# Kernel tuning notes

Hardware: AMD Instinct MI355X
Metric: run time of the kernel (lower is better)

The kernel has to match this reference:

```python
import jax, jax.numpy as jnp
import numpy as np

B, C_IN, C_OUT, H, W, OH, OW, K = 2, 8, 16, 512, 1024, 512, 1024, 9


def setup_inputs() -> dict:
    key = jax.random.key(0)
    k1, k2, k3, k4 = jax.random.split(key, 4)
    x = jax.random.normal(k1, (B, C_IN, H, W), dtype=jnp.float32)
    # sample_map holds (x, y) float pixel coords; scale rand [0,1) into bounds
    sm = jax.random.uniform(k2, (OH, OW, K, 2), dtype=jnp.float32)
    sample_map = sm * jnp.array([W - 1.0, H - 1.0], dtype=jnp.float32)
    n = C_IN * K
    stdv = 1.0 / np.sqrt(n)
    weight = jax.random.uniform(k3, (C_OUT, C_IN, K), dtype=jnp.float32,
                                minval=-stdv, maxval=stdv)
    bias = jax.random.uniform(k4, (C_OUT,), dtype=jnp.float32,
                              minval=-stdv, maxval=stdv)
    return {"x": x, "sample_map": sample_map, "weight": weight, "bias": bias}


def _bilinear_sample(x, sample_map):
    # x: [B,C,H,W]; sample_map: [OH,OW,K,2] with (px, py)
    b, c, h, w = x.shape
    px = sample_map[..., 0]  # [OH,OW,K]
    py = sample_map[..., 1]
    x0 = jnp.floor(px)
    y0 = jnp.floor(py)
    wx = px - x0
    wy = py - y0
    x0i = jnp.clip(x0.astype(jnp.int32), 0, w - 1)
    x1i = jnp.clip(x0i + 1, 0, w - 1)
    y0i = jnp.clip(y0.astype(jnp.int32), 0, h - 1)
    y1i = jnp.clip(y0i + 1, 0, h - 1)
    x_flat = x.reshape(b, c, h * w)

    def gather(yi, xi):
        flat = (yi * w + xi).reshape(-1)
        g = jnp.take(x_flat, flat, axis=2)
        return g.reshape(b, c, *yi.shape)  # [B,C,OH,OW,K]

    wx = wx[None, None]
    wy = wy[None, None]
    sampled = ((1 - wy) * (1 - wx) * gather(y0i, x0i)
               + (1 - wy) * wx * gather(y0i, x1i)
               + wy * (1 - wx) * gather(y1i, x0i)
               + wy * wx * gather(y1i, x1i))
    return sampled  # [B,C,OH,OW,K]


def reference(x, sample_map, weight, bias):
    sampled = _bilinear_sample(x, sample_map)          # [B,C,OH,OW,K]
    out = jnp.einsum('bchwk,ock->bohw', sampled, weight)
    return out + bias[None, :, None, None]
```

## Files before the change

kernel.cpp:

```cpp
#include <hip/hip_runtime.h>

#define BB   2
#define CIN  8
#define COUT 16
#define HH   512
#define WW   1024
#define KK   9
#define NPIX (HH*WW)
#define COPY4 (1u << 20)

typedef unsigned int u32;
typedef float f32x4 __attribute__((ext_vector_type(4)));
typedef float f32x2 __attribute__((ext_vector_type(2)));

#define SB() __builtin_amdgcn_sched_barrier(0)

__device__ __forceinline__ u32 f2bf(float f) {
  u32 u = __float_as_uint(f);
  return (u + 0x7fffu + ((u >> 16) & 1u)) >> 16;
}
__device__ __forceinline__ float bflo(u32 u) { return __uint_as_float(u << 16); }
__device__ __forceinline__ float bfhi(u32 u) { return __uint_as_float(u & 0xffff0000u); }
__device__ __forceinline__ u32 comp4(uint4 v, int j) {
  return j == 0 ? v.x : j == 1 ? v.y : j == 2 ? v.z : v.w;
}


__global__ __launch_bounds__(256) void xpose3c_k(const float* __restrict__ x,
                                                 uint4* __restrict__ xt4) {
  int t = blockIdx.x * 256 + threadIdx.x;
  if (t >= (HH / 2) * (WW / 2) * BB) return;
  int b  = t & 1;
  int s  = t >> 1;
  int by = s >> 9;
  int bx = s & 511;

  u32 pk[3][3][4];
  #pragma unroll
  for (int j = 0; j < 4; ++j) {
    const float* c0 = x + (size_t)(b * CIN + 2 * j    ) * NPIX;
    const float* c1 = x + (size_t)(b * CIN + 2 * j + 1) * NPIX;
    int i1 = min(bx + 1, WW / 2 - 1);
    #pragma unroll
    for (int r = 0; r < 3; ++r) {
      int row = min(2 * by + r, HH - 1);
      const float2* p0 = (const float2*)(c0 + (size_t)row * WW);
      const float2* p1 = (const float2*)(c1 + (size_t)row * WW);
      float2 a0 = p0[bx], a1 = p0[i1];
      float2 b0 = p1[bx], b1 = p1[i1];
      pk[r][0][j] = f2bf(a0.x) | (f2bf(b0.x) << 16);
      pk[r][1][j] = f2bf(a0.y) | (f2bf(b0.y) << 16);
      pk[r][2][j] = f2bf(a1.x) | (f2bf(b1.x) << 16);
    }
  }

  #pragma unroll
  for (int pyp = 0; pyp < 2; ++pyp)
    #pragma unroll
    for (int pxp = 0; pxp < 2; ++pxp) {
      u32 base = ((u32)(pyp * 2 + pxp) << 20)
               + ((u32)(by * 512 + bx) * 2 + (u32)b) * 4;
      #pragma unroll
      for (int d = 0; d < 4; ++d) {
        int dy = d >> 1, dx = d & 1;
        uint4 v;
        v.x = pk[pyp + dy][pxp + dx][0];
        v.y = pk[pyp + dy][pxp + dx][1];
        v.z = pk[pyp + dy][pxp + dx][2];
        v.w = pk[pyp + dy][pxp + dx][3];
        xt4[base + d] = v;
      }
    }
}

__global__ __launch_bounds__(256) void mconv6_k(const uint4* __restrict__ xt4,
                                                const float* __restrict__ sm,
                                                const float* __restrict__ weight,
                                                const float* __restrict__ bias,
                                                float* __restrict__ out) {
  __shared__ float sml[128 * KK * 2];
  __shared__ float wlds[KK * CIN * COUT];

  int tid = threadIdx.x;
  {
    const f32x4* g = (const f32x4*)(sm + (size_t)blockIdx.x * 128 * KK * 2);
    f32x4* l = (f32x4*)sml;
    for (int i = tid; i < 128 * KK * 2 / 4; i += 256) l[i] = g[i];
  }
  for (int i = tid; i < KK * CIN * COUT; i += 256) {
    int k = i >> 7, c = (i >> 4) & 7, o = i & 15;
    wlds[i] = weight[(o * CIN + c) * KK + k];
  }
  __syncthreads();

  const int pl = tid & 127;
  const int b  = tid >> 7;
  const int p  = blockIdx.x * 128 + pl;

  f32x2 acc2[8];
  #pragma unroll
  for (int o2 = 0; o2 < 8; ++o2) { acc2[o2][0] = bias[2*o2]; acc2[o2][1] = bias[2*o2+1]; }

  const float2* smp = (const float2*)sml + pl * KK;

  auto LOADK = [&](int k, uint4 (&v)[4]) {
    float2 s = smp[k];
    int x0 = min(max((int)floorf(s.x), 0), WW - 2);
    int y0 = min(max((int)floorf(s.y), 0), HH - 2);
    u32 idx = ((u32)((y0 & 1) * 2 + (x0 & 1)) << 20)
            + ((u32)((y0 >> 1) * 512 + (x0 >> 1)) * 2 + (u32)b) * 4;
    v[0] = xt4[idx];     v[1] = xt4[idx + 1];
    v[2] = xt4[idx + 2]; v[3] = xt4[idx + 3];
  };

  auto CONS = [&](int k, uint4 (&v)[4]) {
    float2 s = smp[k];
    float x0f = floorf(s.x), y0f = floorf(s.y);
    float wx = s.x - x0f, wy = s.y - y0f;
    float w00 = (1.f - wy) * (1.f - wx), w01 = (1.f - wy) * wx;
    float w10 = wy * (1.f - wx),         w11 = wy * wx;
    const float4* w4 = (const float4*)&wlds[k * (CIN * COUT)];

    float sv[8];
    #pragma unroll
    for (int j = 0; j < 4; ++j) {
      u32 a00 = comp4(v[0], j), a01 = comp4(v[1], j);
      u32 a10 = comp4(v[2], j), a11 = comp4(v[3], j);
      sv[2*j]   = w00*bflo(a00) + w01*bflo(a01) + w10*bflo(a10) + w11*bflo(a11);
      sv[2*j+1] = w00*bfhi(a00) + w01*bfhi(a01) + w10*bfhi(a10) + w11*bfhi(a11);
    }
    #pragma unroll
    for (int c = 0; c < 8; ++c) {
      float s0 = sv[c];
      #pragma unroll
      for (int og = 0; og < 4; ++og) {
        float4 wv = w4[c * 4 + og];
        f32x2 wlo; wlo[0] = wv.x; wlo[1] = wv.y;
        f32x2 whi; whi[0] = wv.z; whi[1] = wv.w;
        acc2[og*2]   += wlo * s0;
        acc2[og*2+1] += whi * s0;
      }
    }
  };

  uint4 va[4], vb[4], vc[4], vd[4];
  LOADK(0, va); LOADK(1, vb); LOADK(2, vc); LOADK(3, vd); SB();
  CONS(0, va);  SB(); LOADK(4, va); SB();
  CONS(1, vb);  SB(); LOADK(5, vb); SB();
  CONS(2, vc);  SB(); LOADK(6, vc); SB();
  CONS(3, vd);  SB(); LOADK(7, vd); SB();
  CONS(4, va);  SB(); LOADK(8, va); SB();
  CONS(5, vb);  SB();
  CONS(6, vc);  SB();
  CONS(7, vd);  SB();
  CONS(8, va);

  #pragma unroll
  for (int o2 = 0; o2 < 8; ++o2) {
    __builtin_nontemporal_store(acc2[o2][0], &out[(size_t)(b * COUT + 2*o2    ) * NPIX + p]);
    __builtin_nontemporal_store(acc2[o2][1], &out[(size_t)(b * COUT + 2*o2 + 1) * NPIX + p]);
  }
}

__global__ __launch_bounds__(256) void mconv_direct_k(const float* __restrict__ x,
                                                      const float* __restrict__ sm,
                                                      const float* __restrict__ weight,
                                                      const float* __restrict__ bias,
                                                      float* __restrict__ out) {
  __shared__ float wlds[KK * CIN * COUT];
  int tid = threadIdx.x;
  for (int i = tid; i < KK * CIN * COUT; i += 256) {
    int k = i >> 7, c = (i >> 4) & 7, o = i & 15;
    wlds[i] = weight[(o * CIN + c) * KK + k];
  }
  __syncthreads();

  int p = blockIdx.x * 256 + tid;
  if (p >= NPIX) return;

  float acc[2][COUT];
  #pragma unroll
  for (int o = 0; o < COUT; ++o) { float bv = bias[o]; acc[0][o] = bv; acc[1][o] = bv; }

  const float2* smp = (const float2*)sm;

  for (int k = 0; k < KK; ++k) {
    float2 s = smp[(size_t)p * KK + k];
    float x0f = floorf(s.x), y0f = floorf(s.y);
    float wx = s.x - x0f, wy = s.y - y0f;
    int x0 = min(max((int)x0f, 0), WW - 1);
    int y0 = min(max((int)y0f, 0), HH - 1);
    int x1 = min(x0 + 1, WW - 1), y1 = min(y0 + 1, HH - 1);
    float w00 = (1.f - wy) * (1.f - wx), w01 = (1.f - wy) * wx;
    float w10 = wy * (1.f - wx),         w11 = wy * wx;

    float sv[2][8];
    #pragma unroll
    for (int b = 0; b < 2; ++b) {
      #pragma unroll
      for (int c = 0; c < 8; ++c) {
        const float* xp = x + (size_t)(b * CIN + c) * NPIX;
        float v00 = xp[y0 * WW + x0], v01 = xp[y0 * WW + x1];
        float v10 = xp[y1 * WW + x0], v11 = xp[y1 * WW + x1];
        sv[b][c] = w00 * v00 + w01 * v01 + w10 * v10 + w11 * v11;
      }
    }

    const float4* w4 = (const float4*)&wlds[k * (CIN * COUT)];
    #pragma unroll
    for (int c = 0; c < 8; ++c) {
      float s0 = sv[0][c], s1 = sv[1][c];
      #pragma unroll
      for (int og = 0; og < 4; ++og) {
        float4 wv = w4[c * 4 + og];
        acc[0][og*4+0] += s0 * wv.x; acc[1][og*4+0] += s1 * wv.x;
        acc[0][og*4+1] += s0 * wv.y; acc[1][og*4+1] += s1 * wv.y;
        acc[0][og*4+2] += s0 * wv.z; acc[1][og*4+2] += s1 * wv.z;
        acc[0][og*4+3] += s0 * wv.w; acc[1][og*4+3] += s1 * wv.w;
      }
    }
  }

  #pragma unroll
  for (int b = 0; b < 2; ++b)
    #pragma unroll
    for (int o = 0; o < COUT; ++o)
      out[(size_t)(b * COUT + o) * NPIX + p] = acc[b][o];
}

extern "C" void kernel_launch(void* const* d_in, const int* in_sizes, int n_in,
                              void* d_out, int out_size, void* d_ws, size_t ws_size,
                              hipStream_t stream) {
  const float* x      = (const float*)d_in[0];
  const float* sm     = (const float*)d_in[1];
  const float* weight = (const float*)d_in[2];
  const float* bias   = (const float*)d_in[3];
  float* out = (float*)d_out;

  const size_t oneCopy = (size_t)COPY4 * sizeof(uint4);
  uint4* xt4 = (uint4*)d_ws;
  if (ws_size >= 4 * oneCopy) {
    hipLaunchKernelGGL(xpose3c_k, dim3((HH / 2) * (WW / 2) * BB / 256), dim3(256), 0,
                       stream, x, xt4);
    hipLaunchKernelGGL(mconv6_k, dim3(NPIX / 128), dim3(256), 0, stream,
                       xt4, sm, weight, bias, out);
  } else {
    hipLaunchKernelGGL(mconv_direct_k, dim3((NPIX + 255) / 256), dim3(256), 0, stream,
                       x, sm, weight, bias, out);
  }
}
```

Before: 141.6 us.

## Deepen gather prefetch with inline-asm loads and explicit vmcnt waits

The gather kernel now issues its global loads through inline assembly, with six taps in flight instead of four. Explicit s_waitcnt vmcnt counts let each tap's bilinear and weight math start as soon as its own data arrives. All nine gather addresses are computed up front, and launch bounds request a minimum occupancy of 3 blocks per CU. The aim is to hide more gather latency through deeper memory-level parallelism, at the cost of more registers, which the occupancy hint may squeeze. Hand-counted vmcnt values are fragile if the compiler emits any other vector-memory ops in between.

```diff
diff --git a/kernel.cpp b/kernel.cpp
--- a/kernel.cpp
+++ b/kernel.cpp
@@ -12,8 +12,7 @@
 typedef unsigned int u32;
 typedef float f32x4 __attribute__((ext_vector_type(4)));
 typedef float f32x2 __attribute__((ext_vector_type(2)));
-
-#define SB() __builtin_amdgcn_sched_barrier(0)
+typedef unsigned int u32x4 __attribute__((ext_vector_type(4)));
 
 __device__ __forceinline__ u32 f2bf(float f) {
   u32 u = __float_as_uint(f);
@@ -21,9 +20,6 @@
 }
 __device__ __forceinline__ float bflo(u32 u) { return __uint_as_float(u << 16); }
 __device__ __forceinline__ float bfhi(u32 u) { return __uint_as_float(u & 0xffff0000u); }
-__device__ __forceinline__ u32 comp4(uint4 v, int j) {
-  return j == 0 ? v.x : j == 1 ? v.y : j == 2 ? v.z : v.w;
-}
 
 
 __global__ __launch_bounds__(256) void xpose3c_k(const float* __restrict__ x,
@@ -73,11 +69,24 @@
     }
 }
 
-__global__ __launch_bounds__(256) void mconv6_k(const uint4* __restrict__ xt4,
-                                                const float* __restrict__ sm,
-                                                const float* __restrict__ weight,
-                                                const float* __restrict__ bias,
-                                                float* __restrict__ out) {
+#define LOADQ(K, B)                                                     \
+  { const u32x4* _a = xbase + iq[K];                                    \
+    asm volatile("global_load_dwordx4 %0, %4, off\n\t"                  \
+                 "global_load_dwordx4 %1, %4, off offset:16\n\t"        \
+                 "global_load_dwordx4 %2, %4, off offset:32\n\t"        \
+                 "global_load_dwordx4 %3, %4, off offset:48"            \
+                 : "=&v"(B##0), "=&v"(B##1), "=&v"(B##2), "=&v"(B##3)   \
+                 : "v"(_a)); }
+
+#define WAITQ(N, B)                                                     \
+  asm volatile("s_waitcnt vmcnt(" #N ")"                                \
+               : "+v"(B##0), "+v"(B##1), "+v"(B##2), "+v"(B##3))
+
+__global__ __launch_bounds__(256, 3) void mconv7_k(const uint4* __restrict__ xt4,
+                                                   const float* __restrict__ sm,
+                                                   const float* __restrict__ weight,
+                                                   const float* __restrict__ bias,
+                                                   float* __restrict__ out) {
   __shared__ float sml[128 * KK * 2];
   __shared__ float wlds[KK * CIN * COUT];
 
@@ -100,20 +109,23 @@
   f32x2 acc2[8];
   #pragma unroll
   for (int o2 = 0; o2 < 8; ++o2) { acc2[o2][0] = bias[2*o2]; acc2[o2][1] = bias[2*o2+1]; }
+  asm volatile("" : "+v"(acc2[0]), "+v"(acc2[1]), "+v"(acc2[2]), "+v"(acc2[3]),
+                    "+v"(acc2[4]), "+v"(acc2[5]), "+v"(acc2[6]), "+v"(acc2[7]));
 
   const float2* smp = (const float2*)sml + pl * KK;
-
-  auto LOADK = [&](int k, uint4 (&v)[4]) {
+  const u32x4* xbase = (const u32x4*)xt4;
+
+  u32 iq[9];
+  #pragma unroll
+  for (int k = 0; k < KK; ++k) {
     float2 s = smp[k];
     int x0 = min(max((int)floorf(s.x), 0), WW - 2);
     int y0 = min(max((int)floorf(s.y), 0), HH - 2);
-    u32 idx = ((u32)((y0 & 1) * 2 + (x0 & 1)) << 20)
-            + ((u32)((y0 >> 1) * 512 + (x0 >> 1)) * 2 + (u32)b) * 4;
-    v[0] = xt4[idx];     v[1] = xt4[idx + 1];
-    v[2] = xt4[idx + 2]; v[3] = xt4[idx + 3];
-  };
-
-  auto CONS = [&](int k, uint4 (&v)[4]) {
+    iq[k] = ((u32)((y0 & 1) * 2 + (x0 & 1)) << 20)
+          + ((u32)((y0 >> 1) * 512 + (x0 >> 1)) * 2 + (u32)b) * 4;
+  }
+
+  auto CONS = [&](int k, u32x4 v0, u32x4 v1, u32x4 v2, u32x4 v3) {
     float2 s = smp[k];
     float x0f = floorf(s.x), y0f = floorf(s.y);
     float wx = s.x - x0f, wy = s.y - y0f;
@@ -124,8 +136,7 @@
     float sv[8];
     #pragma unroll
     for (int j = 0; j < 4; ++j) {
-      u32 a00 = comp4(v[0], j), a01 = comp4(v[1], j);
-      u32 a10 = comp4(v[2], j), a11 = comp4(v[3], j);
+      u32 a00 = v0[j], a01 = v1[j], a10 = v2[j], a11 = v3[j];
       sv[2*j]   = w00*bflo(a00) + w01*bflo(a01) + w10*bflo(a10) + w11*bflo(a11);
       sv[2*j+1] = w00*bfhi(a00) + w01*bfhi(a01) + w10*bfhi(a10) + w11*bfhi(a11);
     }
@@ -143,17 +154,17 @@
     }
   };
 
-  uint4 va[4], vb[4], vc[4], vd[4];
-  LOADK(0, va); LOADK(1, vb); LOADK(2, vc); LOADK(3, vd); SB();
-  CONS(0, va);  SB(); LOADK(4, va); SB();
-  CONS(1, vb);  SB(); LOADK(5, vb); SB();
-  CONS(2, vc);  SB(); LOADK(6, vc); SB();
-  CONS(3, vd);  SB(); LOADK(7, vd); SB();
-  CONS(4, va);  SB(); LOADK(8, va); SB();
-  CONS(5, vb);  SB();
-  CONS(6, vc);  SB();
-  CONS(7, vd);  SB();
-  CONS(8, va);
+  u32x4 A0,A1,A2,A3, B0,B1,B2,B3, C0,C1,C2,C3, D0,D1,D2,D3, E0,E1,E2,E3, F0,F1,F2,F3;
+  LOADQ(0, A); LOADQ(1, B); LOADQ(2, C); LOADQ(3, D); LOADQ(4, E); LOADQ(5, F);
+  WAITQ(20, A); CONS(0, A0,A1,A2,A3); LOADQ(6, A);
+  WAITQ(20, B); CONS(1, B0,B1,B2,B3); LOADQ(7, B);
+  WAITQ(20, C); CONS(2, C0,C1,C2,C3); LOADQ(8, C);
+  WAITQ(20, D); CONS(3, D0,D1,D2,D3);
+  WAITQ(16, E); CONS(4, E0,E1,E2,E3);
+  WAITQ(12, F); CONS(5, F0,F1,F2,F3);
+  WAITQ( 8, A); CONS(6, A0,A1,A2,A3);
+  WAITQ( 4, B); CONS(7, B0,B1,B2,B3);
+  WAITQ( 0, C); CONS(8, C0,C1,C2,C3);
 
   #pragma unroll
   for (int o2 = 0; o2 < 8; ++o2) {
@@ -242,7 +253,7 @@
   if (ws_size >= 4 * oneCopy) {
     hipLaunchKernelGGL(xpose3c_k, dim3((HH / 2) * (WW / 2) * BB / 256), dim3(256), 0,
                        stream, x, xt4);
-    hipLaunchKernelGGL(mconv6_k, dim3(NPIX / 128), dim3(256), 0, stream,
+    hipLaunchKernelGGL(mconv7_k, dim3(NPIX / 128), dim3(256), 0, stream,
                        xt4, sm, weight, bias, out);
   } else {
     hipLaunchKernelGGL(mconv_direct_k, dim3((NPIX + 255) / 256), dim3(256), 0, stream,
```

Result: slower. 149.5 us (+5.5%).

## Process both batches per thread to share sample-map decode and index math

Applied to the files above, without the earlier changes.

Each thread now handles one pixel for both batch elements, reading 8 contiguous uint4 (both batches' 2x2 neighbourhoods) per tap instead of splitting the batch across half the threads. Sample coordinates and gather indices are decoded once per pixel and kept in registers, bilinear weights are shared, the pipeline becomes double-buffered with 8-wide loads, and the sample map is read with nontemporal loads. Accumulators double to 32 floats per thread and launch bounds request 4 waves per SIMD. The cost is higher register pressure and fewer loads in flight per stage.

```diff
diff --git a/kernel.cpp b/kernel.cpp
--- a/kernel.cpp
+++ b/kernel.cpp
@@ -73,19 +73,20 @@
     }
 }
 
-__global__ __launch_bounds__(256) void mconv6_k(const uint4* __restrict__ xt4,
-                                                const float* __restrict__ sm,
-                                                const float* __restrict__ weight,
-                                                const float* __restrict__ bias,
-                                                float* __restrict__ out) {
-  __shared__ float sml[128 * KK * 2];
+__global__ __launch_bounds__(256, 4) void mconv8_k(const uint4* __restrict__ xt4,
+                                                   const float* __restrict__ sm,
+                                                   const float* __restrict__ weight,
+                                                   const float* __restrict__ bias,
+                                                   float* __restrict__ out) {
+  __shared__ float sml[256 * KK * 2];
   __shared__ float wlds[KK * CIN * COUT];
 
   int tid = threadIdx.x;
   {
-    const f32x4* g = (const f32x4*)(sm + (size_t)blockIdx.x * 128 * KK * 2);
+    const f32x4* g = (const f32x4*)(sm + (size_t)blockIdx.x * 256 * KK * 2);
     f32x4* l = (f32x4*)sml;
-    for (int i = tid; i < 128 * KK * 2 / 4; i += 256) l[i] = g[i];
+    for (int i = tid; i < 256 * KK * 2 / 4; i += 256)
+      l[i] = __builtin_nontemporal_load(g + i);
   }
   for (int i = tid; i < KK * CIN * COUT; i += 256) {
     int k = i >> 7, c = (i >> 4) & 7, o = i & 15;
@@ -93,27 +94,34 @@
   }
   __syncthreads();
 
-  const int pl = tid & 127;
-  const int b  = tid >> 7;
-  const int p  = blockIdx.x * 128 + pl;
-
-  f32x2 acc2[8];
-  #pragma unroll
-  for (int o2 = 0; o2 < 8; ++o2) { acc2[o2][0] = bias[2*o2]; acc2[o2][1] = bias[2*o2+1]; }
-
-  const float2* smp = (const float2*)sml + pl * KK;
-
-  auto LOADK = [&](int k, uint4 (&v)[4]) {
+  const int p = blockIdx.x * 256 + tid;
+
+  f32x2 acc2[16];
+  #pragma unroll
+  for (int o2 = 0; o2 < 8; ++o2) {
+    f32x2 bv; bv[0] = bias[2*o2]; bv[1] = bias[2*o2+1];
+    acc2[o2] = bv; acc2[8 + o2] = bv;
+  }
+
+  const float2* smp = (const float2*)sml + tid * KK;
+
+  u32 iq[9];
+  #pragma unroll
+  for (int k = 0; k < KK; ++k) {
     float2 s = smp[k];
     int x0 = min(max((int)floorf(s.x), 0), WW - 2);
     int y0 = min(max((int)floorf(s.y), 0), HH - 2);
-    u32 idx = ((u32)((y0 & 1) * 2 + (x0 & 1)) << 20)
-            + ((u32)((y0 >> 1) * 512 + (x0 >> 1)) * 2 + (u32)b) * 4;
-    v[0] = xt4[idx];     v[1] = xt4[idx + 1];
-    v[2] = xt4[idx + 2]; v[3] = xt4[idx + 3];
+    iq[k] = ((u32)((y0 & 1) * 2 + (x0 & 1)) << 20)
+          + ((u32)((y0 >> 1) * 512 + (x0 >> 1)) * 8);
+  }
+
+  auto LOADK = [&](int k, uint4 (&v)[8]) {
+    const uint4* a = xt4 + iq[k];
+    #pragma unroll
+    for (int j = 0; j < 8; ++j) v[j] = a[j];
   };
 
-  auto CONS = [&](int k, uint4 (&v)[4]) {
+  auto CONS = [&](int k, uint4 (&v)[8]) {
     float2 s = smp[k];
     float x0f = floorf(s.x), y0f = floorf(s.y);
     float wx = s.x - x0f, wy = s.y - y0f;
@@ -121,45 +129,50 @@
     float w10 = wy * (1.f - wx),         w11 = wy * wx;
     const float4* w4 = (const float4*)&wlds[k * (CIN * COUT)];
 
-    float sv[8];
-    #pragma unroll
-    for (int j = 0; j < 4; ++j) {
-      u32 a00 = comp4(v[0], j), a01 = comp4(v[1], j);
-      u32 a10 = comp4(v[2], j), a11 = comp4(v[3], j);
-      sv[2*j]   = w00*bflo(a00) + w01*bflo(a01) + w10*bflo(a10) + w11*bflo(a11);
-      sv[2*j+1] = w00*bfhi(a00) + w01*bfhi(a01) + w10*bfhi(a10) + w11*bfhi(a11);
-    }
-    #pragma unroll
-    for (int c = 0; c < 8; ++c) {
-      float s0 = sv[c];
-      #pragma unroll
-      for (int og = 0; og < 4; ++og) {
-        float4 wv = w4[c * 4 + og];
-        f32x2 wlo; wlo[0] = wv.x; wlo[1] = wv.y;
-        f32x2 whi; whi[0] = wv.z; whi[1] = wv.w;
-        acc2[og*2]   += wlo * s0;
-        acc2[og*2+1] += whi * s0;
+    #pragma unroll
+    for (int b = 0; b < 2; ++b) {
+      float sv[8];
+      #pragma unroll
+      for (int j = 0; j < 4; ++j) {
+        u32 a00 = comp4(v[4*b+0], j), a01 = comp4(v[4*b+1], j);
+        u32 a10 = comp4(v[4*b+2], j), a11 = comp4(v[4*b+3], j);
+        sv[2*j]   = w00*bflo(a00) + w01*bflo(a01) + w10*bflo(a10) + w11*bflo(a11);
+        sv[2*j+1] = w00*bfhi(a00) + w01*bfhi(a01) + w10*bfhi(a10) + w11*bfhi(a11);
+      }
+      #pragma unroll
+      for (int c = 0; c < 8; ++c) {
+        float s0 = sv[c];
+        #pragma unroll
+        for (int og = 0; og < 4; ++og) {
+          float4 wv = w4[c * 4 + og];
+          f32x2 wlo; wlo[0] = wv.x; wlo[1] = wv.y;
+          f32x2 whi; whi[0] = wv.z; whi[1] = wv.w;
+          acc2[b*8 + og*2]     += wlo * s0;
+          acc2[b*8 + og*2 + 1] += whi * s0;
+        }
       }
     }
   };
 
-  uint4 va[4], vb[4], vc[4], vd[4];
-  LOADK(0, va); LOADK(1, vb); LOADK(2, vc); LOADK(3, vd); SB();
-  CONS(0, va);  SB(); LOADK(4, va); SB();
-  CONS(1, vb);  SB(); LOADK(5, vb); SB();
-  CONS(2, vc);  SB(); LOADK(6, vc); SB();
-  CONS(3, vd);  SB(); LOADK(7, vd); SB();
-  CONS(4, va);  SB(); LOADK(8, va); SB();
-  CONS(5, vb);  SB();
-  CONS(6, vc);  SB();
-  CONS(7, vd);  SB();
+  uint4 va[8], vb[8];
+  LOADK(0, va); SB(); LOADK(1, vb); SB();
+  CONS(0, va);  SB(); LOADK(2, va); SB();
+  CONS(1, vb);  SB(); LOADK(3, vb); SB();
+  CONS(2, va);  SB(); LOADK(4, va); SB();
+  CONS(3, vb);  SB(); LOADK(5, vb); SB();
+  CONS(4, va);  SB(); LOADK(6, va); SB();
+  CONS(5, vb);  SB(); LOADK(7, vb); SB();
+  CONS(6, va);  SB(); LOADK(8, va); SB();
+  CONS(7, vb);  SB();
   CONS(8, va);
 
   #pragma unroll
-  for (int o2 = 0; o2 < 8; ++o2) {
-    __builtin_nontemporal_store(acc2[o2][0], &out[(size_t)(b * COUT + 2*o2    ) * NPIX + p]);
-    __builtin_nontemporal_store(acc2[o2][1], &out[(size_t)(b * COUT + 2*o2 + 1) * NPIX + p]);
-  }
+  for (int b = 0; b < 2; ++b)
+    #pragma unroll
+    for (int o2 = 0; o2 < 8; ++o2) {
+      __builtin_nontemporal_store(acc2[b*8+o2][0], &out[(size_t)(b * COUT + 2*o2    ) * NPIX + p]);
+      __builtin_nontemporal_store(acc2[b*8+o2][1], &out[(size_t)(b * COUT + 2*o2 + 1) * NPIX + p]);
+    }
 }
 
 __global__ __launch_bounds__(256) void mconv_direct_k(const float* __restrict__ x,
@@ -242,7 +255,7 @@
   if (ws_size >= 4 * oneCopy) {
     hipLaunchKernelGGL(xpose3c_k, dim3((HH / 2) * (WW / 2) * BB / 256), dim3(256), 0,
                        stream, x, xt4);
-    hipLaunchKernelGGL(mconv6_k, dim3(NPIX / 128), dim3(256), 0, stream,
+    hipLaunchKernelGGL(mconv8_k, dim3(NPIX / 256), dim3(256), 0, stream,
                        xt4, sm, weight, bias, out);
   } else {
     hipLaunchKernelGGL(mconv_direct_k, dim3((NPIX + 255) / 256), dim3(256), 0, stream,
```

New measurement: 363.3 us. +156.6%, slower.
